# Kernel optimization log

Hardware: AMD Instinct MI355X
Metric: run time of the kernel (lower is better)

## Reference

```python
import jax, jax.numpy as jnp
import numpy as np

DT = 1.0
EPS = 1e-6


def setup_inputs() -> dict:
    key = jax.random.key(0)
    ks = jax.random.split(key, 5)
    B, I, H = 8192, 512, 1024
    scale = (6.0 / ((1 + 5.0) * (I + H))) ** 0.5  # kaiming_uniform with a=sqrt(5) bound
    return {
        "x": jax.random.normal(ks[0], (B, I), dtype=jnp.float32),
        "hidden": jax.random.normal(ks[1], (B, H), dtype=jnp.float32),
        "W_tau": jax.random.uniform(ks[2], (H, I + H), dtype=jnp.float32, minval=-scale, maxval=scale),
        "b_tau": jnp.zeros((H,), dtype=jnp.float32),
        "W_r": jax.random.uniform(ks[3], (H, I + H), dtype=jnp.float32, minval=-scale, maxval=scale),
        "b_r": jnp.zeros((H,), dtype=jnp.float32),
        "W_h": jax.random.uniform(ks[4], (H, I + H), dtype=jnp.float32, minval=-scale, maxval=scale),
        "b_h": jnp.zeros((H,), dtype=jnp.float32),
    }


def reference(x, hidden, W_tau, b_tau, W_r, b_r, W_h, b_h):
    combined = jnp.concatenate([x, hidden], axis=1)          # [B, I+H]
    tau = jax.nn.softplus(combined @ W_tau.T + b_tau) + EPS  # [B, H]
    r = jax.nn.sigmoid(combined @ W_r.T + b_r)               # [B, H]
    gated = r * hidden
    cand_in = jnp.concatenate([x, gated], axis=1)            # [B, I+H]
    h_tilde = jnp.tanh(cand_in @ W_h.T + b_h)                # [B, H]
    return hidden + DT * (h_tilde - hidden) / tau
```

## Files before the change

### kernel.cpp

```cpp
#include <hip/hip_runtime.h>
#include <hip/hip_bf16.h>

typedef __attribute__((ext_vector_type(8))) unsigned short u16x8;
typedef __attribute__((ext_vector_type(8))) __bf16        bf16x8;
typedef __attribute__((ext_vector_type(4))) float         f32x4;

static constexpr int B_ = 8192;
static constexpr int I_ = 512;
static constexpr int H_ = 1024;
static constexpr int K_ = 1536;
static constexpr int NT    = K_ / 64;
static constexpr int NITER = NT / 2;

#define AS1 __attribute__((address_space(1)))
#define AS3 __attribute__((address_space(3)))

__device__ __forceinline__ unsigned short f2bf(float f) {
    unsigned int u = __float_as_uint(f);
    u += 0x7FFF + ((u >> 16) & 1);
    return (unsigned short)(u >> 16);
}
__device__ __forceinline__ float bf2f(unsigned short u) {
    return __uint_as_float(((unsigned int)u) << 16);
}

__device__ __forceinline__ void memfence() { asm volatile("" ::: "memory"); }
__device__ __forceinline__ void barrier_() {
    memfence(); __builtin_amdgcn_s_barrier(); memfence();
}
__device__ __forceinline__ void vwait6() {
    asm volatile("s_waitcnt vmcnt(6)" ::: "memory");
    __builtin_amdgcn_sched_barrier(0);
}
__device__ __forceinline__ void vwait0() {
    asm volatile("s_waitcnt vmcnt(0)" ::: "memory");
    __builtin_amdgcn_sched_barrier(0);
}

__device__ __forceinline__ u16x8 cvt8(const float4* s) {
    float4 a = s[0], b = s[1];
    u16x8 o;
    o[0] = f2bf(a.x); o[1] = f2bf(a.y); o[2] = f2bf(a.z); o[3] = f2bf(a.w);
    o[4] = f2bf(b.x); o[5] = f2bf(b.y); o[6] = f2bf(b.z); o[7] = f2bf(b.w);
    return o;
}

__global__ void prep(const float* __restrict__ x, const float* __restrict__ hid,
                     const float* __restrict__ wt, const float* __restrict__ wr,
                     const float* __restrict__ wh,
                     unsigned short* __restrict__ cmb1,
                     unsigned short* __restrict__ wtb,
                     unsigned short* __restrict__ wrb,
                     unsigned short* __restrict__ whb) {
    constexpr int NX8 = B_ * I_ / 8;
    constexpr int NH8 = B_ * H_ / 8;
    constexpr int NW8 = H_ * K_ / 8;
    int i = blockIdx.x * blockDim.x + threadIdx.x;
    if (i < NX8) {
        int row = i >> 6, c8 = i & 63;
        u16x8 o = cvt8((const float4*)x + (size_t)i * 2);
        *(u16x8*)(cmb1 + (size_t)row * K_ + c8 * 8) = o;
    } else if (i < NX8 + NH8) {
        int j = i - NX8;
        int row = j >> 7, c8 = j & 127;
        u16x8 o = cvt8((const float4*)hid + (size_t)j * 2);
        *(u16x8*)(cmb1 + (size_t)row * K_ + 512 + c8 * 8) = o;
    } else {
        int k = i - (NX8 + NH8);
        const float* src; unsigned short* dst;
        if (k < NW8)          { src = wt; dst = wtb; }
        else if (k < 2 * NW8) { src = wr; dst = wrb; k -= NW8; }
        else                  { src = wh; dst = whb; k -= 2 * NW8; }
        u16x8 o = cvt8((const float4*)src + (size_t)k * 2);
        *(u16x8*)(dst + (size_t)k * 8) = o;
    }
}

__global__ __launch_bounds__(512, 1)
void gemm_tr(const unsigned short* __restrict__ A,
             const unsigned short* __restrict__ W0,
             const unsigned short* __restrict__ W1,
             const float* __restrict__ b0,
             const float* __restrict__ b1,
             const float* __restrict__ hidden,
             unsigned short* __restrict__ itau_out,
             unsigned short* __restrict__ gate_out)
{
    extern __shared__ __align__(16) char lds[];

    const int t = threadIdx.x;
    const int w = t >> 6, l = t & 63;
    const int wg  = blockIdx.y * 8 + blockIdx.x;
    const int swz = (wg & 7) * 32 + (wg >> 3);
    const int m0  = (swz >> 3) * 256;
    const int n0  = (swz & 7) * 128;

    const int srow  = t >> 3;
    const int sslot = ((t & 7) ^ (srow & 7)) * 8;
    const unsigned short* srcA  = A  + (size_t)(m0 + srow) * K_ + sslot;
    const unsigned short* srcB0 = W0 + (size_t)(n0 + srow) * K_ + sslot;
    const unsigned short* srcB1 = W1 + (size_t)(n0 + srow) * K_ + sslot;
    char* dstA = lds + w * 1024;
    char* dstB = lds + 65536 + w * 1024;

    auto stageA = [&](int tt) {
        const unsigned short* s = srcA + tt * 64;
        char* d = dstA + (tt & 1) * 32768;
        #pragma unroll
        for (int q = 0; q < 4; ++q)
            __builtin_amdgcn_global_load_lds(
                (const AS1 void*)(s + (size_t)q * 64 * K_),
                (AS3 void*)(d + q * 8192), 16, 0, 0);
    };
    auto stageB = [&](int tt, int wi) {
        const unsigned short* s = (wi ? srcB1 : srcB0) + tt * 64;
        char* d = dstB + (tt & 1) * 32768 + wi * 16384;
        #pragma unroll
        for (int h = 0; h < 2; ++h)
            __builtin_amdgcn_global_load_lds(
                (const AS1 void*)(s + (size_t)(h * 64) * K_),
                (AS3 void*)(d + h * 8192), 16, 0, 0);
    };

    const int fr = l & 15, kq = l >> 4;
    const int wm = w >> 1, wn = w & 1;
    const int fx = (kq ^ (fr & 7)) << 4;
    const char* rdA0 = lds + (wm * 32 + fr) * 128 + fx;
    const char* rdA1 = lds + (wm * 32 + fr) * 128 + (fx ^ 64);
    const char* rdB0 = lds + 65536 + (wn * 32 + fr) * 128 + fx;
    const char* rdB1 = lds + 65536 + (wn * 32 + fr) * 128 + (fx ^ 64);

    bf16x8 af[4][2], bfr[2][2][2];
    f32x4 acc[2][4][4];
    #pragma unroll
    for (int wi = 0; wi < 2; ++wi)
        #pragma unroll
        for (int i = 0; i < 4; ++i)
            #pragma unroll
            for (int jn = 0; jn < 4; ++jn) acc[wi][i][jn] = (f32x4)0.0f;

    auto readAfull = [&](int par) {
        #pragma unroll
        for (int mf = 0; mf < 4; ++mf) {
            const int off = par * 32768 + (mf >> 1) * 16384 + (mf & 1) * 2048;
            af[mf][0] = *(const bf16x8*)(rdA0 + off);
            af[mf][1] = *(const bf16x8*)(rdA1 + off);
        }
    };
    auto readB = [&](int wi, int par) {
        #pragma unroll
        for (int bh = 0; bh < 2; ++bh)
            #pragma unroll
            for (int ni = 0; ni < 2; ++ni) {
                const int off = par * 32768 + wi * 16384 + bh * 8192 + ni * 2048;
                bfr[bh][ni][0] = *(const bf16x8*)(rdB0 + off);
                bfr[bh][ni][1] = *(const bf16x8*)(rdB1 + off);
            }
    };
    auto mfma32 = [&](int wi) {
        __builtin_amdgcn_s_setprio(1);
        #pragma unroll
        for (int mf = 0; mf < 4; ++mf)
            #pragma unroll
            for (int bh = 0; bh < 2; ++bh)
                #pragma unroll
                for (int ni = 0; ni < 2; ++ni)
                    #pragma unroll
                    for (int ks = 0; ks < 2; ++ks)
                        acc[wi][mf][bh * 2 + ni] =
                            __builtin_amdgcn_mfma_f32_16x16x32_bf16(
                                af[mf][ks], bfr[bh][ni][ks],
                                acc[wi][mf][bh * 2 + ni], 0, 0, 0);
        __builtin_amdgcn_s_setprio(0);
    };

    stageA(0); stageB(0, 0); stageB(0, 1);
    stageA(1); stageB(1, 0);
    vwait6(); barrier_();

    for (int j = 0; j < NITER; ++j) {
        const int tE = (2 * j + 2 < NT) ? 2 * j + 2 : 0;
        const int tO = (2 * j + 3 < NT) ? 2 * j + 3 : 0;
        readAfull(0); readB(0, 0); stageB(2 * j + 1, 1);
        mfma32(0); barrier_();
        readB(1, 0); stageA(tE); stageB(tE, 0);
        mfma32(1); vwait6(); barrier_();
        readAfull(1); readB(0, 1); stageB(tE, 1);
        mfma32(0); barrier_();
        readB(1, 1); stageA(tO); stageB(tO, 0);
        mfma32(1); vwait6(); barrier_();
    }
    vwait0();

    const int rs4 = kq * 4;
    const int nB0 = n0 + wn * 32;
    #pragma unroll
    for (int wi = 0; wi < 2; ++wi)
        #pragma unroll
        for (int mf = 0; mf < 4; ++mf)
            #pragma unroll
            for (int bh = 0; bh < 2; ++bh)
                #pragma unroll
                for (int ni = 0; ni < 2; ++ni) {
                    const int n = nB0 + bh * 64 + ni * 16 + fr;
                    const float bv = (wi ? b1 : b0)[n];
                    #pragma unroll
                    for (int jj = 0; jj < 4; ++jj) {
                        const int m = m0 + (mf >> 1) * 128 + wm * 32 + (mf & 1) * 16 + rs4 + jj;
                        const size_t ix = (size_t)m * H_ + n;
                        const float z = acc[wi][mf][bh * 2 + ni][jj] + bv;
                        if (wi == 0) {
                            const float sp = (z > 15.f) ? z : __logf(1.0f + __expf(z));
                            itau_out[ix] = f2bf(__fdividef(1.0f, sp + 1e-6f));
                        } else {
                            const float r = __fdividef(1.0f, 1.0f + __expf(-z));
                            gate_out[(size_t)m * K_ + 512 + n] = f2bf(r * hidden[ix]);
                        }
                    }
                }
}

__global__ __launch_bounds__(256, 2)
void gemm_h(const unsigned short* __restrict__ A1,
            const unsigned short* __restrict__ A2,
            const unsigned short* __restrict__ W,
            const float* __restrict__ bias,
            const float* __restrict__ hidden,
            const unsigned short* __restrict__ itau_in,
            float* __restrict__ outF)
{
    extern __shared__ __align__(16) char lds[];

    const int t = threadIdx.x;
    const int w = t >> 6, l = t & 63;
    const int wg  = blockIdx.y * 8 + blockIdx.x;
    const int swz = (wg & 7) * 64 + (wg >> 3);
    const int m0  = (swz >> 3) * 128;
    const int n0  = (swz & 7) * 128;

    const int srow  = t >> 3;
    const int sslot = ((t & 7) ^ (srow & 7)) * 8;
    const unsigned short* srcA1 = A1 + (size_t)(m0 + srow) * K_ + sslot;
    const unsigned short* srcA2 = A2 + (size_t)(m0 + srow) * K_ + sslot;
    const unsigned short* srcB  = W  + (size_t)(n0 + srow) * K_ + sslot;

    auto stageTile = [&](int bi, int ts) {
        const unsigned short* sA = (ts >= 8 ? srcA2 : srcA1) + ts * 64;
        char* dA = lds + bi * 16384 + w * 1024;
        #pragma unroll
        for (int q = 0; q < 4; ++q)
            __builtin_amdgcn_global_load_lds(
                (const AS1 void*)(sA + (size_t)q * 32 * K_),
                (AS3 void*)(dA + q * 4096), 16, 0, 0);
        const unsigned short* sB = srcB + ts * 64;
        char* dB = lds + 32768 + bi * 16384 + w * 1024;
        #pragma unroll
        for (int q = 0; q < 4; ++q)
            __builtin_amdgcn_global_load_lds(
                (const AS1 void*)(sB + (size_t)q * 32 * K_),
                (AS3 void*)(dB + q * 4096), 16, 0, 0);
    };

    const int fr = l & 15, kq = l >> 4;
    const int wm = w >> 1, wn = w & 1;
    const int fx = (kq ^ (fr & 7)) << 4;
    const char* rdA0 = lds + (wm * 64 + fr) * 128 + fx;
    const char* rdA1 = lds + (wm * 64 + fr) * 128 + (fx ^ 64);
    const char* rdB0 = lds + 32768 + (wn * 64 + fr) * 128 + fx;
    const char* rdB1 = lds + 32768 + (wn * 64 + fr) * 128 + (fx ^ 64);

    bf16x8 af[4][2], bfr[4][2];
    f32x4 acc[4][4];
    #pragma unroll
    for (int i = 0; i < 4; ++i)
        #pragma unroll
        for (int jn = 0; jn < 4; ++jn) acc[i][jn] = (f32x4)0.0f;

    auto readFrags = [&](int bi) {
        #pragma unroll
        for (int mf = 0; mf < 4; ++mf) {
            af[mf][0] = *(const bf16x8*)(rdA0 + bi * 16384 + mf * 2048);
            af[mf][1] = *(const bf16x8*)(rdA1 + bi * 16384 + mf * 2048);
        }
        #pragma unroll
        for (int nf = 0; nf < 4; ++nf) {
            bfr[nf][0] = *(const bf16x8*)(rdB0 + bi * 16384 + nf * 2048);
            bfr[nf][1] = *(const bf16x8*)(rdB1 + bi * 16384 + nf * 2048);
        }
    };
    auto mfma32 = [&]() {
        __builtin_amdgcn_s_setprio(1);
        #pragma unroll
        for (int mf = 0; mf < 4; ++mf)
            #pragma unroll
            for (int nf = 0; nf < 4; ++nf)
                #pragma unroll
                for (int ks = 0; ks < 2; ++ks)
                    acc[mf][nf] = __builtin_amdgcn_mfma_f32_16x16x32_bf16(
                        af[mf][ks], bfr[nf][ks], acc[mf][nf], 0, 0, 0);
        __builtin_amdgcn_s_setprio(0);
    };

    stageTile(0, 0);
    vwait0(); barrier_();

    for (int ts = 0; ts < NT; ++ts) {
        const int bi = ts & 1;
        stageTile(bi ^ 1, (ts + 1 < NT) ? ts + 1 : 0);
        readFrags(bi);
        mfma32();
        vwait0(); barrier_();
    }

    const int rs4 = kq * 4;
    #pragma unroll
    for (int mf = 0; mf < 4; ++mf)
        #pragma unroll
        for (int nf = 0; nf < 4; ++nf) {
            const int n = n0 + wn * 64 + nf * 16 + fr;
            const float bv = bias[n];
            #pragma unroll
            for (int jj = 0; jj < 4; ++jj) {
                const int m = m0 + wm * 64 + mf * 16 + rs4 + jj;
                const size_t ix = (size_t)m * H_ + n;
                const float z = acc[mf][nf][jj] + bv;
                const float e2 = __expf(2.0f * z);
                const float th = __fdividef(e2 - 1.0f, e2 + 1.0f);
                const float h = hidden[ix];
                const float it = bf2f(itau_in[ix]);
                outF[ix] = h + (th - h) * it;
            }
        }
}

extern "C" void kernel_launch(void* const* d_in, const int* in_sizes, int n_in,
                              void* d_out, int out_size, void* d_ws, size_t ws_size,
                              hipStream_t stream) {
    (void)in_sizes; (void)n_in; (void)out_size; (void)ws_size;

    const float* x     = (const float*)d_in[0];
    const float* hid   = (const float*)d_in[1];
    const float* W_tau = (const float*)d_in[2];
    const float* b_tau = (const float*)d_in[3];
    const float* W_r   = (const float*)d_in[4];
    const float* b_r   = (const float*)d_in[5];
    const float* W_h   = (const float*)d_in[6];
    const float* b_h   = (const float*)d_in[7];

    unsigned short* cmb1 = (unsigned short*)d_ws;
    unsigned short* cmb2 = cmb1 + (size_t)B_ * K_;
    unsigned short* wtb  = cmb2 + (size_t)B_ * K_;
    unsigned short* wrb  = wtb  + (size_t)H_ * K_;
    unsigned short* whb  = wrb  + (size_t)H_ * K_;
    unsigned short* itau = whb  + (size_t)H_ * K_;

    hipFuncSetAttribute(reinterpret_cast<const void*>(&gemm_tr),
                        hipFuncAttributeMaxDynamicSharedMemorySize, 131072);
    hipFuncSetAttribute(reinterpret_cast<const void*>(&gemm_h),
                        hipFuncAttributeMaxDynamicSharedMemorySize, 65536);

    const int th = 256;
    constexpr int NPREP = B_ * I_ / 8 + B_ * H_ / 8 + 3 * H_ * K_ / 8;
    prep<<<NPREP / th, th, 0, stream>>>(x, hid, W_tau, W_r, W_h,
                                        cmb1, wtb, wrb, whb);

    dim3 g0(8, 32);
    gemm_tr<<<g0, 512, 131072, stream>>>(cmb1, wtb, wrb, b_tau, b_r, hid,
                                         itau, cmb2);
    dim3 g1(8, 64);
    gemm_h<<<g1, 256, 65536, stream>>>(cmb1, cmb2, whb, b_h, hid, itau,
                                       (float*)d_out);
}
```

Measured before the change: 106.1 us.

## Split fused tau/r GEMM into two templated single-weight GEMM launches

The fused kernel that computed both the tau and r projections per tile, sharing each A tile across two weight matrices, is replaced by a templated single-weight kernel launched twice (MODE 0 for tau, MODE 1 for the r gate). Each launch holds half the accumulators and uses less LDS (96KB instead of 128KB), and the pipeline is reorganised into half-A quads with a vmcnt(4) wait. The likely aim is lower register pressure and a simpler schedule. In exchange the shared activation matrix is streamed from memory twice and an extra kernel launch is added.

```diff
diff --git a/kernel.cpp b/kernel.cpp
--- a/kernel.cpp
+++ b/kernel.cpp
@@ -28,8 +28,8 @@
 __device__ __forceinline__ void barrier_() {
     memfence(); __builtin_amdgcn_s_barrier(); memfence();
 }
-__device__ __forceinline__ void vwait6() {
-    asm volatile("s_waitcnt vmcnt(6)" ::: "memory");
+__device__ __forceinline__ void vwait4() {
+    asm volatile("s_waitcnt vmcnt(4)" ::: "memory");
     __builtin_amdgcn_sched_barrier(0);
 }
 __device__ __forceinline__ void vwait0() {
@@ -76,15 +76,14 @@
     }
 }
 
+template<int MODE>
 __global__ __launch_bounds__(512, 1)
-void gemm_tr(const unsigned short* __restrict__ A,
-             const unsigned short* __restrict__ W0,
-             const unsigned short* __restrict__ W1,
-             const float* __restrict__ b0,
-             const float* __restrict__ b1,
-             const float* __restrict__ hidden,
-             unsigned short* __restrict__ itau_out,
-             unsigned short* __restrict__ gate_out)
+void gemm4(const unsigned short* __restrict__ A1,
+           const unsigned short* __restrict__ W0,
+           const float* __restrict__ bias0,
+           const float* __restrict__ hidden,
+           unsigned short* __restrict__ itau_out,
+           unsigned short* __restrict__ gate_out)
 {
     extern __shared__ __align__(16) char lds[];
 
@@ -97,29 +96,24 @@
 
     const int srow  = t >> 3;
     const int sslot = ((t & 7) ^ (srow & 7)) * 8;
-    const unsigned short* srcA  = A  + (size_t)(m0 + srow) * K_ + sslot;
-    const unsigned short* srcB0 = W0 + (size_t)(n0 + srow) * K_ + sslot;
-    const unsigned short* srcB1 = W1 + (size_t)(n0 + srow) * K_ + sslot;
+    const unsigned short* srcA1 = A1 + (size_t)(m0 + srow) * K_ + sslot;
+    const unsigned short* srcB  = W0 + (size_t)(n0 + srow) * K_ + sslot;
     char* dstA = lds + w * 1024;
     char* dstB = lds + 65536 + w * 1024;
 
-    auto stageA = [&](int tt) {
-        const unsigned short* s = srcA + tt * 64;
-        char* d = dstA + (tt & 1) * 32768;
-        #pragma unroll
-        for (int q = 0; q < 4; ++q)
+    auto stageA = [&](int tt, int h) {
+        const unsigned short* s = srcA1 + (size_t)(h * 128) * K_ + tt * 64;
+        char* d = dstA + (tt & 1) * 32768 + h * 16384;
+        #pragma unroll
+        for (int j = 0; j < 2; ++j)
             __builtin_amdgcn_global_load_lds(
-                (const AS1 void*)(s + (size_t)q * 64 * K_),
-                (AS3 void*)(d + q * 8192), 16, 0, 0);
-    };
-    auto stageB = [&](int tt, int wi) {
-        const unsigned short* s = (wi ? srcB1 : srcB0) + tt * 64;
-        char* d = dstB + (tt & 1) * 32768 + wi * 16384;
-        #pragma unroll
-        for (int h = 0; h < 2; ++h)
-            __builtin_amdgcn_global_load_lds(
-                (const AS1 void*)(s + (size_t)(h * 64) * K_),
-                (AS3 void*)(d + h * 8192), 16, 0, 0);
+                (const AS1 void*)(s + (size_t)j * 64 * K_),
+                (AS3 void*)(d + j * 8192), 16, 0, 0);
+    };
+    auto stageB = [&](int tt, int h) {
+        const unsigned short* s = srcB + (size_t)(h * 64) * K_ + tt * 64;
+        char* d = dstB + (tt & 1) * 16384 + h * 8192;
+        __builtin_amdgcn_global_load_lds((const AS1 void*)s, (AS3 void*)d, 16, 0, 0);
     };
 
     const int fr = l & 15, kq = l >> 4;
@@ -130,86 +124,83 @@
     const char* rdB0 = lds + 65536 + (wn * 32 + fr) * 128 + fx;
     const char* rdB1 = lds + 65536 + (wn * 32 + fr) * 128 + (fx ^ 64);
 
-    bf16x8 af[4][2], bfr[2][2][2];
-    f32x4 acc[2][4][4];
+    bf16x8 af[2][2], bfr[2][2][2];
+    f32x4 acc[4][4];
     #pragma unroll
-    for (int wi = 0; wi < 2; ++wi)
-        #pragma unroll
-        for (int i = 0; i < 4; ++i)
-            #pragma unroll
-            for (int jn = 0; jn < 4; ++jn) acc[wi][i][jn] = (f32x4)0.0f;
-
-    auto readAfull = [&](int par) {
-        #pragma unroll
-        for (int mf = 0; mf < 4; ++mf) {
-            const int off = par * 32768 + (mf >> 1) * 16384 + (mf & 1) * 2048;
-            af[mf][0] = *(const bf16x8*)(rdA0 + off);
-            af[mf][1] = *(const bf16x8*)(rdA1 + off);
+    for (int i = 0; i < 4; ++i)
+        #pragma unroll
+        for (int jn = 0; jn < 4; ++jn) acc[i][jn] = (f32x4)0.0f;
+
+    auto readA = [&](int half, int par) {
+        #pragma unroll
+        for (int mi = 0; mi < 2; ++mi) {
+            af[mi][0] = *(const bf16x8*)(rdA0 + par * 32768 + half * 16384 + mi * 2048);
+            af[mi][1] = *(const bf16x8*)(rdA1 + par * 32768 + half * 16384 + mi * 2048);
         }
     };
-    auto readB = [&](int wi, int par) {
+    auto readBall = [&](int par) {
         #pragma unroll
         for (int bh = 0; bh < 2; ++bh)
             #pragma unroll
             for (int ni = 0; ni < 2; ++ni) {
-                const int off = par * 32768 + wi * 16384 + bh * 8192 + ni * 2048;
-                bfr[bh][ni][0] = *(const bf16x8*)(rdB0 + off);
-                bfr[bh][ni][1] = *(const bf16x8*)(rdB1 + off);
+                bfr[bh][ni][0] = *(const bf16x8*)(rdB0 + par * 16384 + bh * 8192 + ni * 2048);
+                bfr[bh][ni][1] = *(const bf16x8*)(rdB1 + par * 16384 + bh * 8192 + ni * 2048);
             }
     };
-    auto mfma32 = [&](int wi) {
+    auto quad16 = [&](int ah) {
         __builtin_amdgcn_s_setprio(1);
         #pragma unroll
-        for (int mf = 0; mf < 4; ++mf)
-            #pragma unroll
-            for (int bh = 0; bh < 2; ++bh)
+        for (int bh = 0; bh < 2; ++bh)
+            #pragma unroll
+            for (int mi = 0; mi < 2; ++mi)
                 #pragma unroll
                 for (int ni = 0; ni < 2; ++ni)
                     #pragma unroll
                     for (int ks = 0; ks < 2; ++ks)
-                        acc[wi][mf][bh * 2 + ni] =
+                        acc[ah * 2 + mi][bh * 2 + ni] =
                             __builtin_amdgcn_mfma_f32_16x16x32_bf16(
-                                af[mf][ks], bfr[bh][ni][ks],
-                                acc[wi][mf][bh * 2 + ni], 0, 0, 0);
+                                af[mi][ks], bfr[bh][ni][ks],
+                                acc[ah * 2 + mi][bh * 2 + ni], 0, 0, 0);
         __builtin_amdgcn_s_setprio(0);
     };
 
-    stageA(0); stageB(0, 0); stageB(0, 1);
-    stageA(1); stageB(1, 0);
-    vwait6(); barrier_();
+    stageA(0, 0); stageA(0, 1); stageB(0, 0); stageB(0, 1);
+    stageA(1, 0); stageB(1, 0); stageB(1, 1);
+    vwait4(); barrier_();
 
     for (int j = 0; j < NITER; ++j) {
         const int tE = (2 * j + 2 < NT) ? 2 * j + 2 : 0;
         const int tO = (2 * j + 3 < NT) ? 2 * j + 3 : 0;
-        readAfull(0); readB(0, 0); stageB(2 * j + 1, 1);
-        mfma32(0); barrier_();
-        readB(1, 0); stageA(tE); stageB(tE, 0);
-        mfma32(1); vwait6(); barrier_();
-        readAfull(1); readB(0, 1); stageB(tE, 1);
-        mfma32(0); barrier_();
-        readB(1, 1); stageA(tO); stageB(tO, 0);
-        mfma32(1); vwait6(); barrier_();
+        readA(0, 0); readBall(0); stageA(2 * j + 1, 1);
+        quad16(0); barrier_();
+        readA(1, 0); stageA(tE, 0); stageB(tE, 0); stageB(tE, 1);
+        quad16(1); vwait4(); barrier_();
+        readA(0, 1); readBall(1); stageA(tE, 1);
+        quad16(0); barrier_();
+        readA(1, 1); stageA(tO, 0); stageB(tO, 0); stageB(tO, 1);
+        quad16(1); vwait4(); barrier_();
     }
     vwait0();
 
     const int rs4 = kq * 4;
     const int nB0 = n0 + wn * 32;
+    const int mB0 = m0 + wm * 32;
     #pragma unroll
-    for (int wi = 0; wi < 2; ++wi)
-        #pragma unroll
-        for (int mf = 0; mf < 4; ++mf)
+    for (int ah = 0; ah < 2; ++ah)
+        #pragma unroll
+        for (int mi = 0; mi < 2; ++mi)
             #pragma unroll
             for (int bh = 0; bh < 2; ++bh)
                 #pragma unroll
                 for (int ni = 0; ni < 2; ++ni) {
                     const int n = nB0 + bh * 64 + ni * 16 + fr;
-                    const float bv = (wi ? b1 : b0)[n];
+                    const float bv = bias0[n];
                     #pragma unroll
                     for (int jj = 0; jj < 4; ++jj) {
-                        const int m = m0 + (mf >> 1) * 128 + wm * 32 + (mf & 1) * 16 + rs4 + jj;
+                        const int m = mB0 + ah * 128 + mi * 16 + rs4 + jj;
                         const size_t ix = (size_t)m * H_ + n;
-                        const float z = acc[wi][mf][bh * 2 + ni][jj] + bv;
-                        if (wi == 0) {
+                        const float z = acc[ah * 2 + mi][bh * 2 + ni][jj] + bv;
+                        if (MODE == 0) {
                             const float sp = (z > 15.f) ? z : __logf(1.0f + __expf(z));
                             itau_out[ix] = f2bf(__fdividef(1.0f, sp + 1e-6f));
                         } else {
@@ -354,8 +345,10 @@
     unsigned short* whb  = wrb  + (size_t)H_ * K_;
     unsigned short* itau = whb  + (size_t)H_ * K_;
 
-    hipFuncSetAttribute(reinterpret_cast<const void*>(&gemm_tr),
-                        hipFuncAttributeMaxDynamicSharedMemorySize, 131072);
+    hipFuncSetAttribute(reinterpret_cast<const void*>(&gemm4<0>),
+                        hipFuncAttributeMaxDynamicSharedMemorySize, 98304);
+    hipFuncSetAttribute(reinterpret_cast<const void*>(&gemm4<1>),
+                        hipFuncAttributeMaxDynamicSharedMemorySize, 98304);
     hipFuncSetAttribute(reinterpret_cast<const void*>(&gemm_h),
                         hipFuncAttributeMaxDynamicSharedMemorySize, 65536);
 
@@ -365,8 +358,8 @@
                                         cmb1, wtb, wrb, whb);
 
     dim3 g0(8, 32);
-    gemm_tr<<<g0, 512, 131072, stream>>>(cmb1, wtb, wrb, b_tau, b_r, hid,
-                                         itau, cmb2);
+    gemm4<0><<<g0, 512, 98304, stream>>>(cmb1, wtb, b_tau, nullptr, itau, nullptr);
+    gemm4<1><<<g0, 512, 98304, stream>>>(cmb1, wrb, b_r, hid, nullptr, cmb2);
     dim3 g1(8, 64);
     gemm_h<<<g1, 256, 65536, stream>>>(cmb1, cmb2, whb, b_h, hid, itau,
                                        (float*)d_out);
```

Result: slower. 112.5 us (+6.0%).
